# Kernel optimization log

Hardware: AMD Instinct MI355X
Metric: run time of the kernel (lower is better)

## Reference

```python
import jax, jax.numpy as jnp
import numpy as np

B, P, S, E, H, NC, NR, NL = 32, 1024, 128, 768, 8, 5, 3, 3


def _adjacency():
    adj = np.zeros((NC, NC, NR), dtype=np.float32)
    for i, j in [(0, 1), (0, 2), (1, 2), (2, 3)]:  # co-occurrence (symmetric)
        adj[i, j, 0] = 1.0
        adj[j, i, 0] = 1.0
    adj[3, 2, 1] = 1.0  # hierarchical
    for i in range(NC):  # self loops
        adj[i, i, 2] = 1.0
    return jnp.asarray(adj)


def _ln(x, g, b, eps=1e-5):
    m = x.mean(-1, keepdims=True)
    v = ((x - m) ** 2).mean(-1, keepdims=True)
    return (x - m) * jax.lax.rsqrt(v + eps) * g + b


def _mha(q, k, v, Wqkv, bqkv, Wo, bo, h=H):
    # torch nn.MultiheadAttention, batch_first=True, eval mode (no dropout),
    # returns (output, attn weights averaged over heads)
    Bq, Lq, Eq = q.shape
    Lk = k.shape[1]
    d = Eq // h
    Wq, Wk, Wv = jnp.split(Wqkv, 3, axis=0)
    bq, bk, bv = jnp.split(bqkv, 3, axis=0)
    qh = (q @ Wq.T + bq).reshape(Bq, Lq, h, d).transpose(0, 2, 1, 3)
    kh = (k @ Wk.T + bk).reshape(Bq, Lk, h, d).transpose(0, 2, 1, 3)
    vh = (v @ Wv.T + bv).reshape(Bq, Lk, h, d).transpose(0, 2, 1, 3)
    scores = jnp.einsum('bhqd,bhkd->bhqk', qh, kh) / jnp.sqrt(jnp.asarray(d, q.dtype))
    a = jax.nn.softmax(scores, axis=-1)
    o = jnp.einsum('bhqk,bhkd->bhqd', a, vh).transpose(0, 2, 1, 3).reshape(Bq, Lq, Eq)
    return o @ Wo.T + bo, a.mean(axis=1)


def setup_inputs() -> dict:
    key = jax.random.key(0)
    ks = iter(jax.random.split(key, 64))
    n = lambda *s: jax.random.normal(next(ks), s, dtype=jnp.float32) * 0.02
    return {
        'visual_features': jax.random.normal(next(ks), (B, P, E), dtype=jnp.float32),
        'text_features': jax.random.normal(next(ks), (B, S, E), dtype=jnp.float32),
        'sentence_embedding': jax.random.normal(next(ks), (B, E), dtype=jnp.float32),
        'class_presence': (jax.random.uniform(next(ks), (B, NC)) > 0.5).astype(jnp.float32),
        # graph layer params stacked over NL layers
        'g_node_emb': n(NL, NC, E), 'g_edge_emb': n(NL, NR, E),
        'g_Wqkv': n(NL, 3 * E, E), 'g_bqkv': jnp.zeros((NL, 3 * E)),
        'g_Wo': n(NL, E, E), 'g_bo': jnp.zeros((NL, E)),
        'g_W1': n(NL, E, 2 * E), 'g_b1': jnp.zeros((NL, E)),
        'g_lng': jnp.ones((NL, E)), 'g_lnb': jnp.zeros((NL, E)),
        'g_W2': n(NL, E, E), 'g_b2': jnp.zeros((NL, E)),
        # visual-text fusion MHA
        'v_Wqkv': n(3 * E, E), 'v_bqkv': jnp.zeros((3 * E,)),
        'v_Wo': n(E, E), 'v_bo': jnp.zeros((E,)),
        # per-class feature generators stacked over NC classes
        'c_W1': n(NC, E, E), 'c_b1': jnp.zeros((NC, E)),
        'c_lng': jnp.ones((NC, E)), 'c_lnb': jnp.zeros((NC, E)),
        'c_W2': n(NC, E, E), 'c_b2': jnp.zeros((NC, E)),
        # global fusion MLP
        'gf_W1': n(E, 2 * E), 'gf_b1': jnp.zeros((E,)),
        'gf_lng': jnp.ones((E,)), 'gf_lnb': jnp.zeros((E,)),
        'gf_W2': n(E, E), 'gf_b2': jnp.zeros((E,)),
        # output proj + final norm
        'out_W': n(E, E), 'out_b': jnp.zeros((E,)),
        'norm_g': jnp.ones((E,)), 'norm_b': jnp.zeros((E,)),
    }


def reference(visual_features, text_features, sentence_embedding, class_presence,
              g_node_emb, g_edge_emb, g_Wqkv, g_bqkv, g_Wo, g_bo, g_W1, g_b1,
              g_lng, g_lnb, g_W2, g_b2, v_Wqkv, v_bqkv, v_Wo, v_bo,
              c_W1, c_b1, c_lng, c_lnb, c_W2, c_b2,
              gf_W1, gf_b1, gf_lng, gf_lnb, gf_W2, gf_b2,
              out_W, out_b, norm_g, norm_b):
    adj = _adjacency()
    Bc = visual_features.shape[0]
    sent = sentence_embedding
    activated, scores = None, None
    for l in range(NL):  # small fixed layer loop
        node_emb = g_node_emb[l]  # [NC, E]
        # sum over relation types of (adj_r @ node_emb) * edge_emb_r, / NR
        edge_feat = jnp.einsum('ijr,je,re->ie', adj, node_emb, g_edge_emb[l]) / NR
        node_f = jnp.broadcast_to(node_emb, (Bc, NC, E))
        combined = jnp.concatenate([node_f, jnp.broadcast_to(edge_feat, (Bc, NC, E))], axis=-1)
        h = combined @ g_W1[l].T + g_b1[l]
        h = jax.nn.relu(_ln(h, g_lng[l], g_lnb[l]))
        updated = h @ g_W2[l].T + g_b2[l]  # [B, NC, E]
        _, w = _mha(sent[:, None, :], updated, updated, g_Wqkv[l], g_bqkv[l], g_Wo[l], g_bo[l])
        scores = jax.nn.softmax(w[:, 0, :] * (class_presence + 0.1), axis=-1)
        activated = updated * scores[..., None]
        sent = sent + activated.mean(axis=1)
    fused, _ = _mha(visual_features, text_features, text_features, v_Wqkv, v_bqkv, v_Wo, v_bo)
    grounded = _ln(visual_features + fused, norm_g, norm_b)
    # grouped per-class MLPs (batched over classes via einsum)
    cf = jnp.einsum('bce,cfe->bcf', activated, c_W1) + c_b1
    cf = jax.nn.relu(_ln(cf, c_lng, c_lnb))
    cf = jnp.einsum('bce,cfe->bcf', cf, c_W2) + c_b2
    gc = jnp.broadcast_to(sent[:, None, :], (Bc, NC, E))
    g = jnp.concatenate([cf, gc], axis=-1) @ gf_W1.T + gf_b1
    g = jax.nn.relu(_ln(g, gf_lng, gf_lnb))
    class_guidance = g @ gf_W2.T + gf_b2
    grounded_out = grounded @ out_W.T + out_b
    return grounded_out, class_guidance, scores
```

## Files before the change

kernel.cpp:

```cpp
#include <hip/hip_runtime.h>
#include <stdint.h>

typedef unsigned short u16;
typedef __attribute__((ext_vector_type(8))) short short8;
typedef __attribute__((ext_vector_type(4))) float f32x4;

#define NB 32
#define PP 1024
#define SEQ 128
#define EE 768
#define HH 8
#define DD 96
#define NCC 5
#define NLL 3

__device__ __forceinline__ float bf2f(u16 x){ unsigned u=((unsigned)x)<<16; float f; __builtin_memcpy(&f,&u,4); return f; }
__device__ __forceinline__ u16 f2bf(float f){ unsigned u; __builtin_memcpy(&u,&f,4); u=(u+0x7FFFu+((u>>16)&1u))>>16; return (u16)u; }

__device__ __forceinline__ short8 cvt8(const float* p) {
  f32x4 a = *(const f32x4*)p;
  f32x4 b = *(const f32x4*)(p+4);
  short8 r;
  r[0]=(short)f2bf(a[0]); r[1]=(short)f2bf(a[1]); r[2]=(short)f2bf(a[2]); r[3]=(short)f2bf(a[3]);
  r[4]=(short)f2bf(b[0]); r[5]=(short)f2bf(b[1]); r[6]=(short)f2bf(b[2]); r[7]=(short)f2bf(b[3]);
  return r;
}

__device__ __forceinline__ void gl16(const u16* g, u16* l) {
  __builtin_amdgcn_global_load_lds((const __attribute__((address_space(1))) void*)g,
                                   (__attribute__((address_space(3))) void*)l, 16, 0, 0);
}

__device__ __forceinline__ const u16* ah_addr(const u16* aBase, int k0) {
  const int h = k0/96;
  return aBase + (size_t)h*98304 + (k0 - h*96);
}

__global__ __launch_bounds__(256) void k_cvt4(
    const float* __restrict__ s0, u16* __restrict__ d0, int c0,
    const float* __restrict__ s1, u16* __restrict__ d1, int c1,
    const float* __restrict__ s2, u16* __restrict__ d2, int c2,
    const float* __restrict__ s3, u16* __restrict__ d3, int c3)
{
  int i = blockIdx.x*256 + threadIdx.x;
  const int stride = gridDim.x*256;
  const int tot = c0+c1+c2+c3;
  for (; i < tot; i += stride) {
    int j = i; const float* s; u16* d;
    if (j < c0) { s=s0; d=d0; }
    else { j-=c0; if (j<c1){s=s1;d=d1;}
      else { j-=c1; if (j<c2){s=s2;d=d2;} else { j-=c2; s=s3; d=d3; } } }
    *(short8*)(d + (size_t)j*8) = cvt8(s + (size_t)j*8);
  }
}

__global__ __launch_bounds__(256) void k_cvt(const float* __restrict__ s, u16* __restrict__ d, int n8) {
  int i = blockIdx.x*256 + threadIdx.x;
  const int stride = gridDim.x*256;
  for (; i < n8; i += stride) *(short8*)(d + (size_t)i*8) = cvt8(s + (size_t)i*8);
}

__device__ __forceinline__ void ln_stats(float v0, float v1, float v2, float* red, int t,
                                         float& mean, float& rstd) {
  float ps = v0+v1+v2;
  float ps2 = v0*v0+v1*v1+v2*v2;
  #pragma unroll
  for (int o=32;o;o>>=1){ ps += __shfl_down(ps,o,64); ps2 += __shfl_down(ps2,o,64); }
  if ((t&63)==0){ red[t>>6]=ps; red[4+(t>>6)]=ps2; }
  __syncthreads();
  mean = (red[0]+red[1]+red[2]+red[3])*(1.0f/EE);
  float var = (red[4]+red[5]+red[6]+red[7])*(1.0f/EE) - mean*mean;
  rstd = rsqrtf(var + 1e-5f);
  __syncthreads();
}

template<int EPI, int AH>
__global__ __launch_bounds__(256) void gemm_bt(const u16* __restrict__ A, const u16* __restrict__ Bw,
        const float* __restrict__ bias, const u16* __restrict__ Res,
        u16* __restrict__ C, float* __restrict__ Cf, u16* __restrict__ C2,
        int M, int N, int K, int NTB)
{
  __shared__ u16 As[2][4096];
  __shared__ u16 Bs[2][4096];
  const int nwg = gridDim.x;
  const int bid = blockIdx.x;
  const int task = (bid & 7)*(nwg >> 3) + (bid >> 3);
  const int m0 = (task / NTB)*128, n0 = (task % NTB)*128;
  const int t = threadIdx.x;
  const int lane = t&63, w = t>>6, wr = w>>1, wc = w&1, lm = lane&15, lg = lane>>4;
  const int o   = w*1024 + lane*16;
  const int srow = o>>6;
  const int sg   = ((o>>4)&3) ^ ((srow>>1)&3);
  const int row0 = m0 + srow;
  const u16* ag    = A + (size_t)row0*K + sg*8;
  const u16* aBase = A + (size_t)((row0>>10)*8)*98304
                       + (size_t)(row0&1023)*96 + sg*8;
  const u16* bg = Bw + (size_t)(n0+srow)*K + sg*8;
  const size_t rstepA = (size_t)64*K;
  const size_t rstepH = 6144;
  const int s  = (lm>>1)&3;
  const int ra = (wr*64+lm)*32 + (lg^s)*8;
  const int rb = (wc*64+lm)*32 + (lg^s)*8;
  const int NT = K>>5;

  f32x4 acc[4][4] = {};
  #pragma unroll
  for (int p=0;p<2;p++) {
    const int k0 = p<<5;
    if constexpr (AH) {
      const u16* pa = ah_addr(aBase, k0);
      gl16(pa,          &As[p][w*512]);
      gl16(pa + rstepH, &As[p][2048 + w*512]);
    } else {
      gl16(ag + k0,          &As[p][w*512]);
      gl16(ag + k0 + rstepA, &As[p][2048 + w*512]);
    }
    gl16(bg + k0,          &Bs[p][w*512]);
    gl16(bg + k0 + rstepA, &Bs[p][2048 + w*512]);
  }
  int cur = 0;
  for (int kt=0; kt<NT; ++kt) {
    if (kt+1 < NT) { asm volatile("s_waitcnt vmcnt(4)" ::: "memory"); }
    else           { asm volatile("s_waitcnt vmcnt(0)" ::: "memory"); }
    __builtin_amdgcn_sched_barrier(0);
    __builtin_amdgcn_s_barrier();
    short8 af[4], bf[4];
    #pragma unroll
    for (int mi=0;mi<4;mi++) af[mi] = *(const short8*)&As[cur][ra + mi*512];
    #pragma unroll
    for (int ni=0;ni<4;ni++) bf[ni] = *(const short8*)&Bs[cur][rb + ni*512];
    asm volatile("s_waitcnt lgkmcnt(0)" ::: "memory");
    __builtin_amdgcn_sched_barrier(0);
    __builtin_amdgcn_s_barrier();
    if (kt+2 < NT) {
      const int k0 = (kt+2)<<5;
      if constexpr (AH) {
        const u16* pa = ah_addr(aBase, k0);
        gl16(pa,          &As[cur][w*512]);
        gl16(pa + rstepH, &As[cur][2048 + w*512]);
      } else {
        gl16(ag + k0,          &As[cur][w*512]);
        gl16(ag + k0 + rstepA, &As[cur][2048 + w*512]);
      }
      gl16(bg + k0,          &Bs[cur][w*512]);
      gl16(bg + k0 + rstepA, &Bs[cur][2048 + w*512]);
    }
    #pragma unroll
    for (int mi=0;mi<4;mi++)
      #pragma unroll
      for (int ni=0;ni<4;ni++)
        acc[mi][ni] = __builtin_amdgcn_mfma_f32_16x16x32_bf16(af[mi], bf[ni], acc[mi][ni], 0,0,0);
    cur ^= 1;
  }
  #pragma unroll
  for (int mi=0;mi<4;mi++) {
    #pragma unroll
    for (int ni=0;ni<4;ni++) {
      const int col = n0 + wc*64 + ni*16 + lm;
      const float bv = bias[col];
      const int hq = (n0 + wc*64 + ni*16)/96;
      const int dq = col - hq*96;
      #pragma unroll
      for (int r=0;r<4;r++) {
        const int row = m0 + wr*64 + mi*16 + lg*4 + r;
        float v = acc[mi][ni][r] + bv;
        if constexpr (EPI==1) v += bf2f(Res[(size_t)row*N + col]);
        if constexpr (EPI==3) {
          Cf[(size_t)row*N + col] = v;
        } else if constexpr (EPI==2) {
          if (col < EE) C[(size_t)row*EE + col] = f2bf(v);
          else C2[((size_t)(row>>7)*EE + (col-EE))*SEQ + (row&127)] = f2bf(v);
        } else if constexpr (EPI==4) {
          C[((size_t)((row>>10)*8 + hq)*1024 + (row&1023))*96 + dq] = f2bf(v);
        } else {
          C[(size_t)row*N + col] = f2bf(v);
        }
      }
    }
  }
}

template<int MT, int AF>
__global__ __launch_bounds__(256) void gemm_tk(const void* __restrict__ Av, const float* __restrict__ W,
    float* __restrict__ Ppart, int ngroups, int KS, int K, int lda, long strideA, long strideW)
{
  const int task = blockIdx.x;
  const int nt = task % 6;
  const int g  = (task/6) % ngroups;
  const int ks = task/(6*ngroups);
  const int t = threadIdx.x, l = t&63, w = t>>6, lm = l&15, lg = l>>4;
  const int slice = K/KS, kbase = ks*slice;
  const int n0 = nt*128 + w*32;
  W += (size_t)g*strideW;
  f32x4 acc[MT/16][2] = {};
  for (int ki=0; ki<slice; ki+=32) {
    const int k0 = kbase + ki;
    short8 af[MT/16];
    #pragma unroll
    for (int m=0;m<MT/16;m++) {
      if constexpr (AF) af[m] = cvt8((const float*)Av + (size_t)g*strideA + (size_t)(m*16+lm)*lda + k0 + lg*8);
      else af[m] = *(const short8*)((const u16*)Av + (size_t)g*strideA + (size_t)(m*16+lm)*lda + k0 + lg*8);
    }
    #pragma unroll
    for (int ni=0;ni<2;ni++) {
      const short8 bf = cvt8(W + (size_t)(n0+ni*16+lm)*K + k0 + lg*8);
      #pragma unroll
      for (int m=0;m<MT/16;m++)
        acc[m][ni] = __builtin_amdgcn_mfma_f32_16x16x32_bf16(af[m], bf, acc[m][ni], 0,0,0);
    }
  }
  float* pb = Ppart + (size_t)(ks*ngroups+g)*MT*768;
  #pragma unroll
  for (int m=0;m<MT/16;m++)
    #pragma unroll
    for (int ni=0;ni<2;ni++)
      #pragma unroll
      for (int r=0;r<4;r++)
        pb[(size_t)(m*16+lg*4+r)*768 + n0+ni*16+lm] = acc[m][ni][r];
}

__global__ __launch_bounds__(256) void k_red(const float* __restrict__ Ppart,
    float* __restrict__ outF, u16* __restrict__ outB,
    const float* __restrict__ bias, long strideB,
    int MT, int ngroups, int KS, int Mreal, long strideR, long strideG)
{
  const int bid = blockIdx.x, g = bid/Mreal, rr = bid%Mreal, t = threadIdx.x;
  #pragma unroll
  for (int i=0;i<3;i++) {
    const int e = t + i*256;
    float s = bias[(size_t)g*strideB + e];
    for (int ks=0; ks<KS; ++ks) s += Ppart[((size_t)(ks*ngroups+g)*MT + rr)*768 + e];
    const size_t off = (size_t)rr*strideR + (size_t)g*strideG + e;
    if (outF) outF[off] = s;
    if (outB) outB[off] = f2bf(s);
  }
}

__global__ __launch_bounds__(256) void k_lnred(const float* __restrict__ Ppart, u16* __restrict__ out,
    const float* __restrict__ bias, long strideB,
    const float* __restrict__ gamma, const float* __restrict__ beta, long strideLn,
    int MT, int ngroups, int KS, int Mreal, long strideR, long strideG)
{
  const int bid = blockIdx.x, g = bid/Mreal, rr = bid%Mreal, t = threadIdx.x;
  __shared__ float red[8];
  float v[3];
  #pragma unroll
  for (int i=0;i<3;i++) {
    const int e = t + i*256;
    float s = bias[(size_t)g*strideB + e];
    for (int ks=0; ks<KS; ++ks) s += Ppart[((size_t)(ks*ngroups+g)*MT + rr)*768 + e];
    v[i] = s;
  }
  float mean, rstd;
  ln_stats(v[0],v[1],v[2], red, t, mean, rstd);
  #pragma unroll
  for (int i=0;i<3;i++) {
    const int e = t + i*256;
    out[(size_t)rr*strideR + (size_t)g*strideG + e] =
        f2bf(fmaxf((v[i]-mean)*rstd*gamma[(size_t)g*strideLn+e]+beta[(size_t)g*strideLn+e], 0.f));
  }
}

__global__ __launch_bounds__(256) void k_comb_si(const float* __restrict__ node_all,
    const float* __restrict__ edge_all, u16* __restrict__ comb,
    const float* __restrict__ se, float* __restrict__ sent)
{
  const int bid = blockIdx.x, t = threadIdx.x;
  if (bid < NLL*NCC) {
    const int ll = bid/NCC, c = bid%NCC;
    const float* node = node_all + (size_t)ll*NCC*EE;
    const float* edge = edge_all + (size_t)ll*3*EE;
    #pragma unroll
    for (int i=0;i<3;i++) {
      const int e = t + i*256;
      float n0=node[e], n1=node[EE+e], n2=node[2*EE+e], n3=node[3*EE+e];
      float nc_=node[(size_t)c*EE+e];
      float e0=edge[e], e1=edge[EE+e], e2=edge[2*EE+e];
      float s0;
      if (c==0) s0=n1+n2; else if (c==1) s0=n0+n2; else if (c==2) s0=n0+n1+n3; else if (c==3) s0=n2; else s0=0.f;
      float ef = (s0*e0 + ((c==3)? n2*e1 : 0.f) + nc_*e2)*(1.0f/3.0f);
      comb[(size_t)bid*2*EE + e]      = f2bf(nc_);
      comb[(size_t)bid*2*EE + EE + e] = f2bf(ef);
    }
  } else {
    const int i = (bid - NLL*NCC)*256 + t;
    if (i < NB*EE) sent[i] = se[i];
  }
}

__global__ __launch_bounds__(256) void k_attn2(int l, const float* __restrict__ qpart,
    const float* __restrict__ bq,
    const float* __restrict__ presence, const float* __restrict__ upd, const float* __restrict__ khg,
    float* __restrict__ sent, float* __restrict__ sc_ws, float* __restrict__ out_scores,
    u16* __restrict__ actB, u16* __restrict__ cat)
{
  const int b = blockIdx.x, t = threadIdx.x;
  __shared__ float qh[EE];
  __shared__ float scl[HH][NCC];
  __shared__ float wsc[NCC];
  __shared__ float scr[NCC];
  #pragma unroll
  for (int i=0;i<3;i++) {
    const int e = t + i*256;
    float s = bq[e];
    #pragma unroll
    for (int ks=0; ks<8; ++ks) s += qpart[((size_t)ks*NB + b)*768 + e];
    qh[e] = s;
  }
  __syncthreads();
  if (t < HH*NCC) {
    const int hh=t/NCC, cc=t%NCC;
    const float* kr = khg + (size_t)(l*NCC+cc)*EE + hh*DD;
    float a=0.f;
    #pragma unroll 8
    for (int d=0;d<DD;d++) a += qh[hh*DD+d]*kr[d];
    scl[hh][cc]=a*0.1020620726159658f;
  }
  __syncthreads();
  if (t < HH) {
    float m=scl[t][0];
    #pragma unroll
    for (int c2=1;c2<NCC;c2++) m=fmaxf(m,scl[t][c2]);
    float ex[NCC]; float s=0.f;
    #pragma unroll
    for (int c2=0;c2<NCC;c2++){ ex[c2]=__expf(scl[t][c2]-m); s+=ex[c2]; }
    #pragma unroll
    for (int c2=0;c2<NCC;c2++) scl[t][c2]=ex[c2]/s;
  }
  __syncthreads();
  if (t < NCC) {
    float wv=0.f;
    #pragma unroll
    for (int hh=0;hh<HH;hh++) wv += scl[hh][t];
    wv *= (1.0f/HH);
    wsc[t] = wv*(presence[b*NCC+t]+0.1f);
  }
  __syncthreads();
  if (t==0) {
    float m=wsc[0];
    #pragma unroll
    for (int c2=1;c2<NCC;c2++) m=fmaxf(m,wsc[c2]);
    float ex[NCC]; float s=0.f;
    #pragma unroll
    for (int c2=0;c2<NCC;c2++){ ex[c2]=__expf(wsc[c2]-m); s+=ex[c2]; }
    #pragma unroll
    for (int c2=0;c2<NCC;c2++){
      float v=ex[c2]/s; scr[c2]=v; sc_ws[b*NCC+c2]=v;
      if (out_scores) out_scores[b*NCC+c2]=v;
    }
  }
  __syncthreads();
  #pragma unroll
  for (int i=0;i<3;i++) {
    const int e=t+i*256;
    float a=0.f;
    #pragma unroll
    for (int c2=0;c2<NCC;c2++) a += scr[c2]*upd[(size_t)(l*NCC+c2)*EE+e];
    const float sn = sent[(size_t)b*EE+e] + a*(1.0f/NCC);
    sent[(size_t)b*EE+e] = sn;
    if (out_scores) {
      const u16 snb = f2bf(sn);
      #pragma unroll
      for (int c2=0;c2<NCC;c2++) {
        actB[((size_t)c2*NB + b)*EE + e] = f2bf(upd[(size_t)(2*NCC+c2)*EE + e]*scr[c2]);
        cat[((size_t)(b*NCC+c2))*2*EE + EE + e] = snb;
      }
    }
  }
}

__global__ __launch_bounds__(256) void attn_k(u16* __restrict__ Q, const u16* __restrict__ Kb,
                                              const u16* __restrict__ Vt)
{
  const int qt = blockIdx.x, h = blockIdx.y, b = blockIdx.z;
  const int t = threadIdx.x, l = t&63, w = t>>6, wr = w>>1, wc = w&1, lm = l&15, lg = l>>4;
  __shared__ u16 Ps[64][136];
  __shared__ float reds[2][64];
  u16* qb = Q + ((size_t)(b*HH+h)*PP + qt*64)*DD;
  const u16* kb = Kb + ((size_t)b*SEQ)*EE + h*DD;
  const u16* vb = Vt + ((size_t)(b*HH+h))*DD*SEQ;

  f32x4 acc[2][4] = {};
  #pragma unroll
  for (int kc=0;kc<3;kc++) {
    short8 af[2], bv[4];
    #pragma unroll
    for (int mi=0;mi<2;mi++) af[mi] = *(const short8*)(qb + (size_t)(wr*32+mi*16+lm)*DD + kc*32 + lg*8);
    #pragma unroll
    for (int ni=0;ni<4;ni++) bv[ni] = *(const short8*)(kb + (size_t)(wc*64+ni*16+lm)*EE + kc*32 + lg*8);
    #pragma unroll
    for (int mi=0;mi<2;mi++)
      #pragma unroll
      for (int ni=0;ni<4;ni++)
        acc[mi][ni] = __builtin_amdgcn_mfma_f32_16x16x32_bf16(af[mi], bv[ni], acc[mi][ni], 0,0,0);
  }
  const float scale = 0.1020620726159658f;
  float gsum[2][4];
  #pragma unroll
  for (int mi=0;mi<2;mi++)
    #pragma unroll
    for (int r=0;r<4;r++) {
      float s=0.f;
      #pragma unroll
      for (int ni=0;ni<4;ni++) {
        float p = __expf(acc[mi][ni][r]*scale);
        acc[mi][ni][r]=p; s+=p;
      }
      #pragma unroll
      for (int mk=1;mk<16;mk<<=1) s += __shfl_xor(s,mk,64);
      gsum[mi][r]=s;
    }
  if (lm==0) {
    #pragma unroll
    for (int mi=0;mi<2;mi++)
      #pragma unroll
      for (int r=0;r<4;r++) reds[wc][wr*32+mi*16+lg*4+r] = gsum[mi][r];
  }
  __syncthreads();
  #pragma unroll
  for (int mi=0;mi<2;mi++)
    #pragma unroll
    for (int r=0;r<4;r++) {
      const int row = wr*32+mi*16+lg*4+r;
      const float inv = 1.0f/(reds[0][row]+reds[1][row]);
      #pragma unroll
      for (int ni=0;ni<4;ni++)
        Ps[row][wc*64+ni*16+lm] = f2bf(acc[mi][ni][r]*inv);
    }
  __syncthreads();

  f32x4 oacc[2][3] = {};
  #pragma unroll
  for (int kc=0;kc<4;kc++) {
    short8 pa[2], vv[3];
    #pragma unroll
    for (int mi=0;mi<2;mi++) pa[mi] = *(const short8*)&Ps[wr*32+mi*16+lm][kc*32+lg*8];
    #pragma unroll
    for (int ni=0;ni<3;ni++) vv[ni] = *(const short8*)(vb + (size_t)(wc*48+ni*16+lm)*SEQ + kc*32 + lg*8);
    #pragma unroll
    for (int mi=0;mi<2;mi++)
      #pragma unroll
      for (int ni=0;ni<3;ni++)
        oacc[mi][ni] = __builtin_amdgcn_mfma_f32_16x16x32_bf16(pa[mi], vv[ni], oacc[mi][ni], 0,0,0);
  }
  #pragma unroll
  for (int mi=0;mi<2;mi++)
    #pragma unroll
    for (int ni=0;ni<3;ni++)
      #pragma unroll
      for (int r=0;r<4;r++)
        qb[(size_t)(wr*32+mi*16+lg*4+r)*DD + wc*48+ni*16+lm] = f2bf(oacc[mi][ni][r]);
}

__global__ __launch_bounds__(256) void k_ln(u16* __restrict__ G, const float* __restrict__ gw, const float* __restrict__ gb)
{
  const int row = blockIdx.x, t = threadIdx.x;
  u16* p = G + (size_t)row*EE;
  __shared__ float red[8];
  float v[3];
  #pragma unroll
  for (int i=0;i<3;i++) v[i]=bf2f(p[t+i*256]);
  float mean, rstd;
  ln_stats(v[0],v[1],v[2], red, t, mean, rstd);
  #pragma unroll
  for (int i=0;i<3;i++) {
    const int e=t+i*256;
    p[e]=f2bf((v[i]-mean)*rstd*gw[e]+gb[e]);
  }
}

extern "C" void kernel_launch(void* const* d_in, const int* in_sizes, int n_in,
                              void* d_out, int out_size, void* d_ws, size_t ws_size,
                              hipStream_t stream)
{
  const float* visual   = (const float*)d_in[0];
  const float* text     = (const float*)d_in[1];
  const float* sentemb  = (const float*)d_in[2];
  const float* presence = (const float*)d_in[3];
  const float* gnode = (const float*)d_in[4];
  const float* gedge = (const float*)d_in[5];
  const float* gWqkv = (const float*)d_in[6];
  const float* gbqkv = (const float*)d_in[7];
  const float* gW1 = (const float*)d_in[10];
  const float* gb1 = (const float*)d_in[11];
  const float* glng = (const float*)d_in[12];
  const float* glnb = (const float*)d_in[13];
  const float* gW2 = (const float*)d_in[14];
  const float* gb2 = (const float*)d_in[15];
  const float* vWqkv = (const float*)d_in[16];
  const float* vbqkv = (const float*)d_in[17];
  const float* vWo = (const float*)d_in[18];
  const float* vbo = (const float*)d_in[19];
  const float* cW1 = (const float*)d_in[20];
  const float* cb1 = (const float*)d_in[21];
  const float* clng = (const float*)d_in[22];
  const float* clnb = (const float*)d_in[23];
  const float* cW2 = (const float*)d_in[24];
  const float* cb2 = (const float*)d_in[25];
  const float* gfW1 = (const float*)d_in[26];
  const float* gfb1 = (const float*)d_in[27];
  const float* gflng = (const float*)d_in[28];
  const float* gflnb = (const float*)d_in[29];
  const float* gfW2 = (const float*)d_in[30];
  const float* gfb2 = (const float*)d_in[31];
  const float* outW = (const float*)d_in[32];
  const float* outb = (const float*)d_in[33];
  const float* normg = (const float*)d_in[34];
  const float* normb = (const float*)d_in[35];

  char* ws = (char*)d_ws;
  u16* wsG   = (u16*)(ws);
  u16* wsK   = (u16*)(ws + 50331648);
  u16* wsVt  = (u16*)(ws + 56623104);
  u16* visB  = (u16*)(ws + 62914560);
  u16* outWB = wsK;

  char* dob = (char*)d_out;
  u16* wsQ    = (u16*)(dob);
  u16* textB  = (u16*)(dob + 50331648);
  u16* WqkvB  = (u16*)(dob + 56623104);
  u16* WoB    = (u16*)(dob + 60162048);
  char* P = dob + 61341696;
  float* wsSent   = (float*)(P);
  float* wsUpd    = (float*)(P +   98304);
  float* wsKhg    = (float*)(P +  144384);
  float* wsScores = (float*)(P +  190464);
  u16*   wsComb   = (u16*)  (P +  191104);
  u16*   wsHb     = (u16*)  (P +  237184);
  u16*   wsUpdB   = (u16*)  (P +  260224);
  u16*   wsActB   = (u16*)  (P +  283264);
  u16*   wsH1b    = (u16*)  (P +  529024);
  u16*   wsCat    = (u16*)  (P +  774784);
  u16*   wsG1b    = (u16*)  (P + 1266304);
  float* Ppart    = (float*)(P + 1512064);

  float* outGO = (float*)d_out;
  float* outCG = outGO + 25165824;
  float* outSC = outGO + 25288704;

  k_cvt4<<<dim3(2048), dim3(256), 0, stream>>>(visual, visB, 3145728,
                                               text, textB, 393216,
                                               vWqkv, WqkvB, 221184,
                                               vWo, WoB, 73728);

  k_comb_si<<<dim3(NLL*NCC + 96), dim3(256), 0, stream>>>(gnode, gedge, wsComb, sentemb, wsSent);
  gemm_tk<16,0><<<dim3(144), dim3(256), 0, stream>>>(wsComb, gW1, Ppart,
      3, 8, 2*EE, 2*EE, (long)NCC*2*EE, (long)EE*2*EE);
  k_lnred<<<dim3(15), dim3(256), 0, stream>>>(Ppart, wsHb, gb1, EE, glng, glnb, EE,
      16, 3, 8, 5, 768, 3840);
  gemm_tk<16,0><<<dim3(72), dim3(256), 0, stream>>>(wsHb, gW2, Ppart,
      3, 4, EE, EE, (long)NCC*EE, (long)EE*EE);
  k_red<<<dim3(15), dim3(256), 0, stream>>>(Ppart, wsUpd, wsUpdB, gb2, EE,
      16, 3, 4, 5, 768, 3840);
  gemm_tk<16,0><<<dim3(72), dim3(256), 0, stream>>>(wsUpdB, gWqkv + (size_t)EE*EE, Ppart,
      3, 4, EE, EE, (long)NCC*EE, (long)3*EE*EE);
  k_red<<<dim3(15), dim3(256), 0, stream>>>(Ppart, wsKhg, nullptr, gbqkv + EE, (long)3*EE,
      16, 3, 4, 5, 768, 3840);

  for (int l=0;l<NLL;l++) {
    gemm_tk<32,1><<<dim3(48), dim3(256), 0, stream>>>(wsSent, gWqkv + (size_t)l*3*EE*EE, Ppart,
        1, 8, EE, EE, 0, 0);
    k_attn2<<<dim3(NB), dim3(256), 0, stream>>>(l, Ppart, gbqkv + (size_t)l*3*EE,
        presence, wsUpd, wsKhg, wsSent, wsScores,
        (l==NLL-1)?outSC:(float*)nullptr, wsActB, wsCat);
  }

  gemm_tk<32,0><<<dim3(120), dim3(256), 0, stream>>>(wsActB, cW1, Ppart,
      5, 4, EE, EE, (long)NB*EE, (long)EE*EE);
  k_lnred<<<dim3(160), dim3(256), 0, stream>>>(Ppart, wsH1b, cb1, EE, clng, clnb, EE,
      32, 5, 4, 32, 768, 24576);
  gemm_tk<32,0><<<dim3(120), dim3(256), 0, stream>>>(wsH1b, cW2, Ppart,
      5, 4, EE, EE, (long)NB*EE, (long)EE*EE);
  k_red<<<dim3(160), dim3(256), 0, stream>>>(Ppart, nullptr, wsCat, cb2, EE,
      32, 5, 4, 32, 7680, 1536);
  gemm_tk<32,0><<<dim3(120), dim3(256), 0, stream>>>(wsCat, gfW1, Ppart,
      5, 4, 2*EE, 2*EE, (long)NB*2*EE, 0);
  k_lnred<<<dim3(160), dim3(256), 0, stream>>>(Ppart, wsG1b, gfb1, 0, gflng, gflnb, 0,
      32, 5, 4, 32, 768, 24576);
  gemm_tk<32,0><<<dim3(120), dim3(256), 0, stream>>>(wsG1b, gfW2, Ppart,
      5, 4, EE, EE, (long)NB*EE, 0);
  k_red<<<dim3(160), dim3(256), 0, stream>>>(Ppart, outCG, nullptr, gfb2, 0,
      32, 5, 4, 32, 768, 24576);

  gemm_bt<4,0><<<dim3(1536), dim3(256), 0, stream>>>(visB, WqkvB, vbqkv, nullptr,
                                                     wsQ, nullptr, nullptr, NB*PP, EE, EE, 6);
  gemm_bt<2,0><<<dim3(384), dim3(256), 0, stream>>>(textB, WqkvB + (size_t)EE*EE, vbqkv+EE, nullptr,
                                                    wsK, nullptr, wsVt, NB*SEQ, 2*EE, EE, 12);
  attn_k<<<dim3(PP/64, HH, NB), dim3(256), 0, stream>>>(wsQ, wsK, wsVt);
  k_cvt<<<dim3(512), dim3(256), 0, stream>>>(outW, outWB, 73728);
  gemm_bt<1,1><<<dim3(1536), dim3(256), 0, stream>>>(wsQ, WoB, vbo, visB,
                                                     wsG, nullptr, nullptr, NB*PP, EE, EE, 6);
  k_ln<<<dim3(NB*PP), dim3(256), 0, stream>>>(wsG, normg, normb);
  gemm_bt<3,0><<<dim3(1536), dim3(256), 0, stream>>>(wsG, outWB, outb, nullptr,
                                                     nullptr, outGO, nullptr, NB*PP, EE, EE, 6);
}
```

Baseline: 457.6 us.

## Keep K/V fragments in registers across eight query tiles per attention block

The attention kernel now processes 512 query rows per block in a loop of eight 64-row tiles. It loads the K and V fragments for a head into registers once instead of once per tile, and prefetches the next Q tile while softmax runs. This cuts redundant K/V global loads and block launch overhead. In exchange the grid shrinks from 4096 to 512 blocks, which may reduce occupancy and latency hiding. Register pressure also rises, and an extra barrier is added per iteration.

```diff
diff --git a/kernel.cpp b/kernel.cpp
--- a/kernel.cpp
+++ b/kernel.cpp
@@ -372,84 +372,107 @@
 __global__ __launch_bounds__(256) void attn_k(u16* __restrict__ Q, const u16* __restrict__ Kb,
                                               const u16* __restrict__ Vt)
 {
-  const int qt = blockIdx.x, h = blockIdx.y, b = blockIdx.z;
+  const int qs = blockIdx.x, h = blockIdx.y, b = blockIdx.z;
   const int t = threadIdx.x, l = t&63, w = t>>6, wr = w>>1, wc = w&1, lm = l&15, lg = l>>4;
   __shared__ u16 Ps[64][136];
   __shared__ float reds[2][64];
-  u16* qb = Q + ((size_t)(b*HH+h)*PP + qt*64)*DD;
   const u16* kb = Kb + ((size_t)b*SEQ)*EE + h*DD;
   const u16* vb = Vt + ((size_t)(b*HH+h))*DD*SEQ;
-
-  f32x4 acc[2][4] = {};
-  #pragma unroll
-  for (int kc=0;kc<3;kc++) {
-    short8 af[2], bv[4];
-    #pragma unroll
-    for (int mi=0;mi<2;mi++) af[mi] = *(const short8*)(qb + (size_t)(wr*32+mi*16+lm)*DD + kc*32 + lg*8);
-    #pragma unroll
-    for (int ni=0;ni<4;ni++) bv[ni] = *(const short8*)(kb + (size_t)(wc*64+ni*16+lm)*EE + kc*32 + lg*8);
+  u16* qbase = Q + ((size_t)(b*HH+h)*PP + (size_t)qs*512)*DD;
+  const float scale = 0.1020620726159658f;
+
+  short8 bv[3][4], vv[4][3];
+  #pragma unroll
+  for (int kc=0;kc<3;kc++)
+    #pragma unroll
+    for (int ni=0;ni<4;ni++)
+      bv[kc][ni] = *(const short8*)(kb + (size_t)(wc*64+ni*16+lm)*EE + kc*32 + lg*8);
+  #pragma unroll
+  for (int kc=0;kc<4;kc++)
+    #pragma unroll
+    for (int ni=0;ni<3;ni++)
+      vv[kc][ni] = *(const short8*)(vb + (size_t)(wc*48+ni*16+lm)*SEQ + kc*32 + lg*8);
+
+  short8 af[3][2];
+  #pragma unroll
+  for (int kc=0;kc<3;kc++)
     #pragma unroll
     for (int mi=0;mi<2;mi++)
-      #pragma unroll
-      for (int ni=0;ni<4;ni++)
-        acc[mi][ni] = __builtin_amdgcn_mfma_f32_16x16x32_bf16(af[mi], bv[ni], acc[mi][ni], 0,0,0);
-  }
-  const float scale = 0.1020620726159658f;
-  float gsum[2][4];
-  #pragma unroll
-  for (int mi=0;mi<2;mi++)
-    #pragma unroll
-    for (int r=0;r<4;r++) {
-      float s=0.f;
-      #pragma unroll
-      for (int ni=0;ni<4;ni++) {
-        float p = __expf(acc[mi][ni][r]*scale);
-        acc[mi][ni][r]=p; s+=p;
+      af[kc][mi] = *(const short8*)(qbase + (size_t)(wr*32+mi*16+lm)*DD + kc*32 + lg*8);
+
+  for (int it=0; it<8; ++it) {
+    u16* qb = qbase + (size_t)it*64*DD;
+    f32x4 acc[2][4] = {};
+    #pragma unroll
+    for (int kc=0;kc<3;kc++)
+      #pragma unroll
+      for (int mi=0;mi<2;mi++)
+        #pragma unroll
+        for (int ni=0;ni<4;ni++)
+          acc[mi][ni] = __builtin_amdgcn_mfma_f32_16x16x32_bf16(af[kc][mi], bv[kc][ni], acc[mi][ni], 0,0,0);
+    if (it < 7) {
+      const u16* qn = qb + (size_t)64*DD;
+      #pragma unroll
+      for (int kc=0;kc<3;kc++)
+        #pragma unroll
+        for (int mi=0;mi<2;mi++)
+          af[kc][mi] = *(const short8*)(qn + (size_t)(wr*32+mi*16+lm)*DD + kc*32 + lg*8);
+    }
+    float gsum[2][4];
+    #pragma unroll
+    for (int mi=0;mi<2;mi++)
+      #pragma unroll
+      for (int r=0;r<4;r++) {
+        float s=0.f;
+        #pragma unroll
+        for (int ni=0;ni<4;ni++) {
+          float p = __expf(acc[mi][ni][r]*scale);
+          acc[mi][ni][r]=p; s+=p;
+        }
+        #pragma unroll
+        for (int mk=1;mk<16;mk<<=1) s += __shfl_xor(s,mk,64);
+        gsum[mi][r]=s;
       }
-      #pragma unroll
-      for (int mk=1;mk<16;mk<<=1) s += __shfl_xor(s,mk,64);
-      gsum[mi][r]=s;
-    }
-  if (lm==0) {
+    if (lm==0) {
+      #pragma unroll
+      for (int mi=0;mi<2;mi++)
+        #pragma unroll
+        for (int r=0;r<4;r++) reds[wc][wr*32+mi*16+lg*4+r] = gsum[mi][r];
+    }
+    __syncthreads();
     #pragma unroll
     for (int mi=0;mi<2;mi++)
       #pragma unroll
-      for (int r=0;r<4;r++) reds[wc][wr*32+mi*16+lg*4+r] = gsum[mi][r];
-  }
-  __syncthreads();
-  #pragma unroll
-  for (int mi=0;mi<2;mi++)
-    #pragma unroll
-    for (int r=0;r<4;r++) {
-      const int row = wr*32+mi*16+lg*4+r;
-      const float inv = 1.0f/(reds[0][row]+reds[1][row]);
-      #pragma unroll
-      for (int ni=0;ni<4;ni++)
-        Ps[row][wc*64+ni*16+lm] = f2bf(acc[mi][ni][r]*inv);
-    }
-  __syncthreads();
-
-  f32x4 oacc[2][3] = {};
-  #pragma unroll
-  for (int kc=0;kc<4;kc++) {
-    short8 pa[2], vv[3];
-    #pragma unroll
-    for (int mi=0;mi<2;mi++) pa[mi] = *(const short8*)&Ps[wr*32+mi*16+lm][kc*32+lg*8];
-    #pragma unroll
-    for (int ni=0;ni<3;ni++) vv[ni] = *(const short8*)(vb + (size_t)(wc*48+ni*16+lm)*SEQ + kc*32 + lg*8);
+      for (int r=0;r<4;r++) {
+        const int row = wr*32+mi*16+lg*4+r;
+        const float inv = 1.0f/(reds[0][row]+reds[1][row]);
+        #pragma unroll
+        for (int ni=0;ni<4;ni++)
+          Ps[row][wc*64+ni*16+lm] = f2bf(acc[mi][ni][r]*inv);
+      }
+    __syncthreads();
+
+    f32x4 oacc[2][3] = {};
+    #pragma unroll
+    for (int kc=0;kc<4;kc++) {
+      short8 pa[2];
+      #pragma unroll
+      for (int mi=0;mi<2;mi++) pa[mi] = *(const short8*)&Ps[wr*32+mi*16+lm][kc*32+lg*8];
+      #pragma unroll
+      for (int mi=0;mi<2;mi++)
+        #pragma unroll
+        for (int ni=0;ni<3;ni++)
+          oacc[mi][ni] = __builtin_amdgcn_mfma_f32_16x16x32_bf16(pa[mi], vv[kc][ni], oacc[mi][ni], 0,0,0);
+    }
     #pragma unroll
     for (int mi=0;mi<2;mi++)
       #pragma unroll
       for (int ni=0;ni<3;ni++)
-        oacc[mi][ni] = __builtin_amdgcn_mfma_f32_16x16x32_bf16(pa[mi], vv[ni], oacc[mi][ni], 0,0,0);
-  }
-  #pragma unroll
-  for (int mi=0;mi<2;mi++)
-    #pragma unroll
-    for (int ni=0;ni<3;ni++)
-      #pragma unroll
-      for (int r=0;r<4;r++)
-        qb[(size_t)(wr*32+mi*16+lg*4+r)*DD + wc*48+ni*16+lm] = f2bf(oacc[mi][ni][r]);
+        #pragma unroll
+        for (int r=0;r<4;r++)
+          qb[(size_t)(wr*32+mi*16+lg*4+r)*DD + wc*48+ni*16+lm] = f2bf(oacc[mi][ni][r]);
+    __syncthreads();
+  }
 }
 
 __global__ __launch_bounds__(256) void k_ln(u16* __restrict__ G, const float* __restrict__ gw, const float* __restrict__ gb)
@@ -586,7 +609,7 @@
                                                      wsQ, nullptr, nullptr, NB*PP, EE, EE, 6);
   gemm_bt<2,0><<<dim3(384), dim3(256), 0, stream>>>(textB, WqkvB + (size_t)EE*EE, vbqkv+EE, nullptr,
                                                     wsK, nullptr, wsVt, NB*SEQ, 2*EE, EE, 12);
-  attn_k<<<dim3(PP/64, HH, NB), dim3(256), 0, stream>>>(wsQ, wsK, wsVt);
+  attn_k<<<dim3(2, HH, NB), dim3(256), 0, stream>>>(wsQ, wsK, wsVt);
   k_cvt<<<dim3(512), dim3(256), 0, stream>>>(outW, outWB, 73728);
   gemm_bt<1,1><<<dim3(1536), dim3(256), 0, stream>>>(wsQ, WoB, vbo, visB,
                                                      wsG, nullptr, nullptr, NB*PP, EE, EE, 6);
```

Measured after the change: 432.9 us (median of 3 runs). 5.4% less time.
